# Optimization experiments

Hardware: AMD Instinct MI355X
Metric: run time of the kernel (lower is better)

## Reference

```python
import jax, jax.numpy as jnp
import numpy as np

B, T, D, U = 64, 2048, 256, 256

def hard_sigmoid(x):
    return jnp.clip(0.2 * x + 0.5, 0.0, 1.0)

def setup_inputs() -> dict:
    key = jax.random.key(0)
    k1, k2, k3 = jax.random.split(key, 3)
    x = jax.random.normal(k1, (B, T, D), dtype=jnp.float32)
    kernel = jax.random.normal(k2, (D, 3 * U), dtype=jnp.float32) * (1.0 / np.sqrt(D))
    recurrent_kernel = jax.random.normal(k3, (U, 3 * U), dtype=jnp.float32) * (1.0 / np.sqrt(U))
    bias = jnp.zeros((3 * U,), dtype=jnp.float32)
    return {"x": x, "kernel": kernel, "recurrent_kernel": recurrent_kernel, "bias": bias}

def reference(x, kernel, recurrent_kernel, bias):
    # implementation=0 style: precompute input projections for all timesteps in one big matmul
    # x: [B,T,D], kernel: [D,3U] -> xz/xr/xh each [B,T,U]
    units = recurrent_kernel.shape[0]
    x_proj = jnp.einsum('btd,dh->bth', x, kernel) + bias  # [B,T,3U]
    xz, xr, xh = jnp.split(x_proj, 3, axis=-1)
    Uz = recurrent_kernel[:, :units]
    Ur = recurrent_kernel[:, units:2 * units]
    Uh = recurrent_kernel[:, 2 * units:]

    def step(h, xs):
        xz_t, xr_t, xh_t = xs  # each [B,U]
        z = hard_sigmoid(xz_t + h @ Uz)
        r = hard_sigmoid(xr_t + h @ Ur)
        hh = jnp.tanh(xh_t + (r * h) @ Uh)
        h_new = z * h + (1.0 - z) * hh
        return h_new, None

    h0 = jnp.zeros((x.shape[0], units), dtype=x.dtype)
    # scan over time: move T to leading axis
    xs = (jnp.swapaxes(xz, 0, 1), jnp.swapaxes(xr, 0, 1), jnp.swapaxes(xh, 0, 1))
    h_last, _ = jax.lax.scan(step, h0, xs)
    return h_last  # [B, U] (return_sequences=False)
```

## Files before the change

kernel.cpp:

```cpp
#include <hip/hip_runtime.h>


#define TB 2048
#define NU 256
#define G3 768

typedef __attribute__((ext_vector_type(8))) short bf16x8;
typedef __attribute__((ext_vector_type(4))) float f32x4;

__device__ inline unsigned short f2bf(float f){
  union{float f; unsigned u;} v; v.f = f;
  unsigned r = v.u + 0x7fffu + ((v.u >> 16) & 1u);
  return (unsigned short)(r >> 16);
}
__device__ inline unsigned pk2(float a, float b){
  return (unsigned)f2bf(a) | ((unsigned)f2bf(b) << 16);
}
__device__ inline float bflo(unsigned u){
  union{unsigned u; float f;} v; v.u = u << 16; return v.f;
}
__device__ inline float bfhi(unsigned u){
  union{unsigned u; float f;} v; v.u = u & 0xffff0000u; return v.f;
}
__device__ inline unsigned cvtpk(float a, float b){
  unsigned r;
  asm("v_cvt_pk_bf16_f32 %0, %1, %2" : "=v"(r) : "v"(a), "v"(b));
  return r;
}
__device__ inline float exp2_fast(float x){
#if __has_builtin(__builtin_amdgcn_exp2f)
  return __builtin_amdgcn_exp2f(x);
#else
  float r; asm("v_exp_f32 %0, %1" : "=v"(r) : "v"(x)); return r;
#endif
}

__global__ __launch_bounds__(256) void transpose_k(const float* __restrict__ W,
                                                   const float* __restrict__ R,
                                                   unsigned short* __restrict__ Wt,
                                                   unsigned short* __restrict__ Ut){
  int n = blockIdx.x;
  int k = threadIdx.x;
  if (n < G3) Wt[n*NU + k] = f2bf(W[k*G3 + n]);
  else        Ut[(n-G3)*NU + k] = f2bf(R[k*G3 + (n-G3)]);
}

__global__ __launch_bounds__(256) void proj_k(const float* __restrict__ x,
                                              const unsigned short* __restrict__ Wt,
                                              const float* __restrict__ bias,
                                              unsigned short* __restrict__ XA,
                                              unsigned short* __restrict__ XB){
  __shared__ short As[4096];
  __shared__ short Bs[4096];
  __shared__ short St[4096];
  const int tid  = threadIdx.x;
  const int lane = tid & 63;
  const int wv   = tid >> 6;
  const int wr   = wv >> 1, wc = wv & 1;
  const int q    = lane >> 4, r16 = lane & 15;
  const int tm   = blockIdx.y;
  const int bn   = blockIdx.x;

  f32x4 acc[2][2];
  #pragma unroll
  for (int a=0;a<2;a++)
    #pragma unroll
    for (int b=0;b<2;b++) acc[a][b] = {0.f,0.f,0.f,0.f};

  const int mA = tid >> 2, kq = tid & 3;
  const int kc32 = kq >> 1, q0 = (kq & 1) * 2;

  for (int kc0 = 0; kc0 < 256; kc0 += 64){
    {
      const float* src = x + (size_t)mA*(2048*256) + (size_t)tm*256 + kc0 + kq*16;
      float4 f0 = *(const float4*)(src);
      float4 f1 = *(const float4*)(src+4);
      float4 f2 = *(const float4*)(src+8);
      float4 f3 = *(const float4*)(src+12);
      *(uint2*)&As[kc32*2048 + q0*512     + mA*8 + 0] = make_uint2(pk2(f0.x,f0.y), pk2(f0.z,f0.w));
      *(uint2*)&As[kc32*2048 + q0*512     + mA*8 + 4] = make_uint2(pk2(f1.x,f1.y), pk2(f1.z,f1.w));
      *(uint2*)&As[kc32*2048 + (q0+1)*512 + mA*8 + 0] = make_uint2(pk2(f2.x,f2.y), pk2(f2.z,f2.w));
      *(uint2*)&As[kc32*2048 + (q0+1)*512 + mA*8 + 4] = make_uint2(pk2(f3.x,f3.y), pk2(f3.z,f3.w));
    }
    {
      const unsigned short* srcB = Wt + (size_t)(bn*64 + mA)*256 + kc0 + kq*16;
      uint4 b0v = *(const uint4*)(srcB);
      uint4 b1v = *(const uint4*)(srcB+8);
      *(uint4*)&Bs[kc32*2048 + q0*512     + mA*8] = b0v;
      *(uint4*)&Bs[kc32*2048 + (q0+1)*512 + mA*8] = b1v;
    }
    __syncthreads();
    #pragma unroll
    for (int kk = 0; kk < 2; kk++){
      bf16x8 av[2], bv[2];
      #pragma unroll
      for (int rt=0; rt<2; rt++)
        av[rt] = *(const bf16x8*)&As[kk*2048 + q*512 + (wr*32+rt*16+r16)*8];
      #pragma unroll
      for (int ct=0; ct<2; ct++)
        bv[ct] = *(const bf16x8*)&Bs[kk*2048 + q*512 + (wc*32+ct*16+r16)*8];
      #pragma unroll
      for (int rt=0; rt<2; rt++)
        #pragma unroll
        for (int ct=0; ct<2; ct++)
          acc[rt][ct] = __builtin_amdgcn_mfma_f32_16x16x32_bf16(av[rt], bv[ct], acc[rt][ct], 0,0,0);
    }
    __syncthreads();
  }

  const int csub = (bn < 4) ? 0 : (bn < 8 ? 256 : 512);
  #pragma unroll
  for (int rt=0; rt<2; rt++){
    #pragma unroll
    for (int ct=0; ct<2; ct++){
      int colg = bn*64 + wc*32 + ct*16 + r16;
      float bb = bias[colg];
      int c = colg - csub;
      int wi = (c >> 5) & 1, tt2 = (c >> 4) & 1, r16g = c & 15;
      #pragma unroll
      for (int i=0;i<4;i++){
        int b = wr*32 + rt*16 + q*4 + i;
        int gg = b >> 4, lb = b & 15;
        int lane_ = (lb >> 2)*16 + r16g, ii = lb & 3;
        St[(gg*2+wi)*512 + lane_*8 + tt2*4 + ii] = (short)f2bf(acc[rt][ct][i] + bb);
      }
    }
  }
  __syncthreads();

  #pragma unroll
  for (int it=0; it<2; it++){
    int idx = tid + it*256;
    int chunk = idx >> 6, within = idx & 63;
    int gg = chunk >> 1, wi = chunk & 1;
    int w_ = (bn & 3)*2 + wi;
    uint4 val = *(const uint4*)&St[chunk*512 + within*8];
    if (bn < 8){
      int sel = (bn < 4) ? 0 : 1;
      *((uint4*)XA + ((((size_t)tm*4+gg)*8 + w_)*64 + within)*2 + sel) = val;
    } else {
      *((uint4*)XB + (((size_t)tm*4+gg)*8 + w_)*64 + within) = val;
    }
  }
}

__global__ __launch_bounds__(512, 2) void gru_k(const unsigned short* __restrict__ XA,
                                                const unsigned short* __restrict__ XB,
                                                const unsigned short* __restrict__ Ut,
                                                float* __restrict__ out){
  __shared__ short fb[8192];

  const int tid  = threadIdx.x;
  const int w    = tid >> 6;
  const int lane = tid & 63;
  const int q    = lane >> 4, r16 = lane & 15;
  const int g    = blockIdx.x;
  const int b0   = g * 16;

  const int lswz = (lane & ~3) | ((lane & 3) ^ ((((lane >> 4) & 1) << 1) | ((lane >> 3) & 1)));
  const int ix   = ((r16 >> 3) << 1) | ((lane >> 5) & 1);
  const int wrb  = w*512 + (r16 >> 3)*128 + q*32 + (r16 & 7);

  for (int i = tid; i < 8192; i += 512) fb[i] = 0;

  bf16x8 Uz[2][8], Ur[2][8], Uh[2][8];
  #pragma unroll
  for (int tt=0; tt<2; tt++){
    int cz = w*32 + tt*16 + r16;
    #pragma unroll
    for (int kc=0; kc<8; kc++){
      Uz[tt][kc] = *(const bf16x8*)&Ut[(cz      )*256 + kc*32 + q*8];
      Ur[tt][kc] = *(const bf16x8*)&Ut[(cz + 256)*256 + kc*32 + q*8];
      Uh[tt][kc] = *(const bf16x8*)&Ut[(cz + 512)*256 + kc*32 + q*8];
    }
  }

  float hprev[2][4] = {{0.f,0.f,0.f,0.f},{0.f,0.f,0.f,0.f}};

  const uint4* pA = (const uint4*)XA + ((size_t)(g*8+w)*64 + lane)*2;
  const uint4* pB = (const uint4*)XB + ((size_t)(g*8+w)*64 + lane);

  uint4 xa0 = pA[0], xa1 = pA[1];
  uint4 xb0 = pB[0];
  pA += 4096; pB += 2048;

  __syncthreads();

  #pragma unroll 1
  for (int t = 0; t < TB; t++){
    uint4 na0 = pA[0], na1 = pA[1];
    uint4 nb0 = pB[0];
    pA += 4096; pB += 2048;

    unsigned xw[8] = {xa0.x,xa0.y,xa0.z,xa0.w,xa1.x,xa1.y,xa1.z,xa1.w};

    f32x4 az[2], ar[2];
    #pragma unroll
    for (int tt=0; tt<2; tt++){
      #pragma unroll
      for (int i=0;i<4;i++){
        int s  = tt*4 + i;
        int sr = 8 + s;
        az[tt][i] = (s&1)  ? bfhi(xw[s>>1])  : bflo(xw[s>>1]);
        ar[tt][i] = (sr&1) ? bfhi(xw[sr>>1]) : bflo(xw[sr>>1]);
      }
    }
    #pragma unroll
    for (int kc=0; kc<8; kc++){
      bf16x8 a = *(const bf16x8*)&fb[kc*512 + lswz*8];
      ar[0] = __builtin_amdgcn_mfma_f32_16x16x32_bf16(a, Ur[0][kc], ar[0], 0,0,0);
      ar[1] = __builtin_amdgcn_mfma_f32_16x16x32_bf16(a, Ur[1][kc], ar[1], 0,0,0);
      az[0] = __builtin_amdgcn_mfma_f32_16x16x32_bf16(a, Uz[0][kc], az[0], 0,0,0);
      az[1] = __builtin_amdgcn_mfma_f32_16x16x32_bf16(a, Uz[1][kc], az[1], 0,0,0);
    }
    #pragma unroll
    for (int tt=0; tt<2; tt++){
      #pragma unroll
      for (int i=0;i<4;i++){
        float rr = __builtin_amdgcn_fmed3f(fmaf(0.2f, ar[tt][i], 0.5f), 0.f, 1.f);
        float v  = rr * hprev[tt][i];
        fb[4096 + wrb + tt*256 + ((i^ix)<<3)] = (short)cvtpk(v, v);
      }
    }
    __syncthreads();

    f32x4 ah[2];
    {
      unsigned xwb[4] = {xb0.x,xb0.y,xb0.z,xb0.w};
      #pragma unroll
      for (int ct=0; ct<2; ct++){
        #pragma unroll
        for (int i=0;i<4;i++){
          int s = ct*4 + i;
          ah[ct][i] = (s&1) ? bfhi(xwb[s>>1]) : bflo(xwb[s>>1]);
        }
      }
    }
    #pragma unroll
    for (int kc=0; kc<8; kc++){
      bf16x8 vv = *(const bf16x8*)&fb[4096 + kc*512 + lswz*8];
      ah[0] = __builtin_amdgcn_mfma_f32_16x16x32_bf16(vv, Uh[0][kc], ah[0], 0,0,0);
      ah[1] = __builtin_amdgcn_mfma_f32_16x16x32_bf16(vv, Uh[1][kc], ah[1], 0,0,0);
    }
    float z8[2][4];
    #pragma unroll
    for (int tt=0; tt<2; tt++)
      #pragma unroll
      for (int i=0;i<4;i++)
        z8[tt][i] = __builtin_amdgcn_fmed3f(fmaf(0.2f, az[tt][i], 0.5f), 0.f, 1.f);
    #pragma unroll
    for (int ct=0; ct<2; ct++){
      #pragma unroll
      for (int i=0;i<4;i++){
        float e  = exp2_fast(2.8853900817779268f * ah[ct][i]);
        float rc = __builtin_amdgcn_rcpf(e + 1.f);
        float hh = fmaf(-2.f, rc, 1.f);
        float hn = fmaf(z8[ct][i], hprev[ct][i] - hh, hh);
        hprev[ct][i] = hn;
        fb[wrb + ct*256 + ((i^ix)<<3)] = (short)cvtpk(hn, hn);
      }
    }
    __syncthreads();

    xa0 = na0; xa1 = na1; xb0 = nb0;
  }

  #pragma unroll
  for (int ct=0; ct<2; ct++)
    #pragma unroll
    for (int i=0;i<4;i++)
      out[(size_t)(b0 + q*4 + i)*256 + w*32 + ct*16 + r16] = hprev[ct][i];
}

extern "C" void kernel_launch(void* const* d_in, const int* in_sizes, int n_in,
                              void* d_out, int out_size, void* d_ws, size_t ws_size,
                              hipStream_t stream) {
  (void)in_sizes; (void)n_in; (void)out_size; (void)ws_size;
  const float* x    = (const float*)d_in[0];
  const float* Wk   = (const float*)d_in[1];
  const float* Rk   = (const float*)d_in[2];
  const float* bias = (const float*)d_in[3];
  float* out = (float*)d_out;

  unsigned short* XA = (unsigned short*)d_ws;
  unsigned short* XB = XA + (size_t)2048*32768;
  unsigned short* Wt = XB + (size_t)2048*16384;
  unsigned short* Ut = Wt + (size_t)768*256;

  hipLaunchKernelGGL(transpose_k, dim3(1536),    dim3(256), 0, stream, Wk, Rk, Wt, Ut);
  hipLaunchKernelGGL(proj_k,      dim3(12,2048), dim3(256), 0, stream, x, Wt, bias, XA, XB);
  hipLaunchKernelGGL(gru_k,       dim3(4),       dim3(512), 0, stream, XA, XB, Ut, out);
}
```

Before: 3.256 ms.

## Keep projection weight tile resident in LDS across 16 timesteps per block

The projection kernel now loads the full 64x256 bf16 weight slice into shared memory once and loops over 16 timesteps per block, cutting the grid from 2048 to 128 blocks along time. This removes repeated weight reloads and per-K-chunk syncs and stages all of K for x at once. In exchange it uses much more LDS per block (about 72KB), which lowers occupancy, and it runs fewer, longer blocks. Total runtime is likely dominated by the sequential GRU kernel, so the gain is limited.

```diff
diff --git a/kernel.cpp b/kernel.cpp
--- a/kernel.cpp
+++ b/kernel.cpp
@@ -50,96 +50,106 @@
                                               const float* __restrict__ bias,
                                               unsigned short* __restrict__ XA,
                                               unsigned short* __restrict__ XB){
-  __shared__ short As[4096];
-  __shared__ short Bs[4096];
+  __shared__ short AsAll[16384];
+  __shared__ short BsAll[16384];
   __shared__ short St[4096];
   const int tid  = threadIdx.x;
   const int lane = tid & 63;
   const int wv   = tid >> 6;
   const int wr   = wv >> 1, wc = wv & 1;
   const int q    = lane >> 4, r16 = lane & 15;
-  const int tm   = blockIdx.y;
   const int bn   = blockIdx.x;
-
-  f32x4 acc[2][2];
-  #pragma unroll
-  for (int a=0;a<2;a++)
-    #pragma unroll
-    for (int b=0;b<2;b++) acc[a][b] = {0.f,0.f,0.f,0.f};
+  const int tc   = blockIdx.y;
 
   const int mA = tid >> 2, kq = tid & 3;
   const int kc32 = kq >> 1, q0 = (kq & 1) * 2;
 
-  for (int kc0 = 0; kc0 < 256; kc0 += 64){
-    {
-      const float* src = x + (size_t)mA*(2048*256) + (size_t)tm*256 + kc0 + kq*16;
+  #pragma unroll
+  for (int kc0i = 0; kc0i < 4; kc0i++){
+    const unsigned short* srcB = Wt + (size_t)(bn*64 + mA)*256 + kc0i*64 + kq*16;
+    uint4 b0v = *(const uint4*)(srcB);
+    uint4 b1v = *(const uint4*)(srcB+8);
+    *(uint4*)&BsAll[kc0i*4096 + kc32*2048 + q0*512     + mA*8] = b0v;
+    *(uint4*)&BsAll[kc0i*4096 + kc32*2048 + (q0+1)*512 + mA*8] = b1v;
+  }
+
+  const int csub = (bn < 4) ? 0 : (bn < 8 ? 256 : 512);
+
+  for (int t16 = 0; t16 < 16; t16++){
+    const int tm = tc*16 + t16;
+
+    #pragma unroll
+    for (int kc0i = 0; kc0i < 4; kc0i++){
+      const float* src = x + (size_t)mA*(2048*256) + (size_t)tm*256 + kc0i*64 + kq*16;
       float4 f0 = *(const float4*)(src);
       float4 f1 = *(const float4*)(src+4);
       float4 f2 = *(const float4*)(src+8);
       float4 f3 = *(const float4*)(src+12);
-      *(uint2*)&As[kc32*2048 + q0*512     + mA*8 + 0] = make_uint2(pk2(f0.x,f0.y), pk2(f0.z,f0.w));
-      *(uint2*)&As[kc32*2048 + q0*512     + mA*8 + 4] = make_uint2(pk2(f1.x,f1.y), pk2(f1.z,f1.w));
-      *(uint2*)&As[kc32*2048 + (q0+1)*512 + mA*8 + 0] = make_uint2(pk2(f2.x,f2.y), pk2(f2.z,f2.w));
-      *(uint2*)&As[kc32*2048 + (q0+1)*512 + mA*8 + 4] = make_uint2(pk2(f3.x,f3.y), pk2(f3.z,f3.w));
-    }
-    {
-      const unsigned short* srcB = Wt + (size_t)(bn*64 + mA)*256 + kc0 + kq*16;
-      uint4 b0v = *(const uint4*)(srcB);
-      uint4 b1v = *(const uint4*)(srcB+8);
-      *(uint4*)&Bs[kc32*2048 + q0*512     + mA*8] = b0v;
-      *(uint4*)&Bs[kc32*2048 + (q0+1)*512 + mA*8] = b1v;
-    }
-    __syncthreads();
-    #pragma unroll
-    for (int kk = 0; kk < 2; kk++){
-      bf16x8 av[2], bv[2];
-      #pragma unroll
-      for (int rt=0; rt<2; rt++)
-        av[rt] = *(const bf16x8*)&As[kk*2048 + q*512 + (wr*32+rt*16+r16)*8];
-      #pragma unroll
-      for (int ct=0; ct<2; ct++)
-        bv[ct] = *(const bf16x8*)&Bs[kk*2048 + q*512 + (wc*32+ct*16+r16)*8];
-      #pragma unroll
-      for (int rt=0; rt<2; rt++)
+      *(uint2*)&AsAll[kc0i*4096 + kc32*2048 + q0*512     + mA*8 + 0] = make_uint2(pk2(f0.x,f0.y), pk2(f0.z,f0.w));
+      *(uint2*)&AsAll[kc0i*4096 + kc32*2048 + q0*512     + mA*8 + 4] = make_uint2(pk2(f1.x,f1.y), pk2(f1.z,f1.w));
+      *(uint2*)&AsAll[kc0i*4096 + kc32*2048 + (q0+1)*512 + mA*8 + 0] = make_uint2(pk2(f2.x,f2.y), pk2(f2.z,f2.w));
+      *(uint2*)&AsAll[kc0i*4096 + kc32*2048 + (q0+1)*512 + mA*8 + 4] = make_uint2(pk2(f3.x,f3.y), pk2(f3.z,f3.w));
+    }
+    __syncthreads();
+
+    f32x4 acc[2][2];
+    #pragma unroll
+    for (int a=0;a<2;a++)
+      #pragma unroll
+      for (int b=0;b<2;b++) acc[a][b] = {0.f,0.f,0.f,0.f};
+
+    #pragma unroll
+    for (int kc0i = 0; kc0i < 4; kc0i++){
+      #pragma unroll
+      for (int kk = 0; kk < 2; kk++){
+        bf16x8 av[2], bv[2];
+        #pragma unroll
+        for (int rt=0; rt<2; rt++)
+          av[rt] = *(const bf16x8*)&AsAll[kc0i*4096 + kk*2048 + q*512 + (wr*32+rt*16+r16)*8];
         #pragma unroll
         for (int ct=0; ct<2; ct++)
-          acc[rt][ct] = __builtin_amdgcn_mfma_f32_16x16x32_bf16(av[rt], bv[ct], acc[rt][ct], 0,0,0);
-    }
-    __syncthreads();
-  }
-
-  const int csub = (bn < 4) ? 0 : (bn < 8 ? 256 : 512);
-  #pragma unroll
-  for (int rt=0; rt<2; rt++){
-    #pragma unroll
-    for (int ct=0; ct<2; ct++){
-      int colg = bn*64 + wc*32 + ct*16 + r16;
-      float bb = bias[colg];
-      int c = colg - csub;
-      int wi = (c >> 5) & 1, tt2 = (c >> 4) & 1, r16g = c & 15;
-      #pragma unroll
-      for (int i=0;i<4;i++){
-        int b = wr*32 + rt*16 + q*4 + i;
-        int gg = b >> 4, lb = b & 15;
-        int lane_ = (lb >> 2)*16 + r16g, ii = lb & 3;
-        St[(gg*2+wi)*512 + lane_*8 + tt2*4 + ii] = (short)f2bf(acc[rt][ct][i] + bb);
-      }
-    }
-  }
-  __syncthreads();
-
-  #pragma unroll
-  for (int it=0; it<2; it++){
-    int idx = tid + it*256;
-    int chunk = idx >> 6, within = idx & 63;
-    int gg = chunk >> 1, wi = chunk & 1;
-    int w_ = (bn & 3)*2 + wi;
-    uint4 val = *(const uint4*)&St[chunk*512 + within*8];
-    if (bn < 8){
-      int sel = (bn < 4) ? 0 : 1;
-      *((uint4*)XA + ((((size_t)tm*4+gg)*8 + w_)*64 + within)*2 + sel) = val;
-    } else {
-      *((uint4*)XB + (((size_t)tm*4+gg)*8 + w_)*64 + within) = val;
+          bv[ct] = *(const bf16x8*)&BsAll[kc0i*4096 + kk*2048 + q*512 + (wc*32+ct*16+r16)*8];
+        #pragma unroll
+        for (int rt=0; rt<2; rt++)
+          #pragma unroll
+          for (int ct=0; ct<2; ct++)
+            acc[rt][ct] = __builtin_amdgcn_mfma_f32_16x16x32_bf16(av[rt], bv[ct], acc[rt][ct], 0,0,0);
+      }
+    }
+    __syncthreads();
+
+    #pragma unroll
+    for (int rt=0; rt<2; rt++){
+      #pragma unroll
+      for (int ct=0; ct<2; ct++){
+        int colg = bn*64 + wc*32 + ct*16 + r16;
+        float bb = bias[colg];
+        int c = colg - csub;
+        int wi = (c >> 5) & 1, tt2 = (c >> 4) & 1, r16g = c & 15;
+        #pragma unroll
+        for (int i=0;i<4;i++){
+          int b = wr*32 + rt*16 + q*4 + i;
+          int gg = b >> 4, lb = b & 15;
+          int lane_ = (lb >> 2)*16 + r16g, ii = lb & 3;
+          St[(gg*2+wi)*512 + lane_*8 + tt2*4 + ii] = (short)f2bf(acc[rt][ct][i] + bb);
+        }
+      }
+    }
+    __syncthreads();
+
+    #pragma unroll
+    for (int it=0; it<2; it++){
+      int idx = tid + it*256;
+      int chunk = idx >> 6, within = idx & 63;
+      int gg = chunk >> 1, wi = chunk & 1;
+      int w_ = (bn & 3)*2 + wi;
+      uint4 val = *(const uint4*)&St[chunk*512 + within*8];
+      if (bn < 8){
+        int sel = (bn < 4) ? 0 : 1;
+        *((uint4*)XA + ((((size_t)tm*4+gg)*8 + w_)*64 + within)*2 + sel) = val;
+      } else {
+        *((uint4*)XB + (((size_t)tm*4+gg)*8 + w_)*64 + within) = val;
+      }
     }
   }
 }
@@ -287,7 +297,7 @@
   unsigned short* Wt = XB + (size_t)2048*16384;
   unsigned short* Ut = Wt + (size_t)768*256;
 
-  hipLaunchKernelGGL(transpose_k, dim3(1536),    dim3(256), 0, stream, Wk, Rk, Wt, Ut);
-  hipLaunchKernelGGL(proj_k,      dim3(12,2048), dim3(256), 0, stream, x, Wt, bias, XA, XB);
-  hipLaunchKernelGGL(gru_k,       dim3(4),       dim3(512), 0, stream, XA, XB, Ut, out);
-}
+  hipLaunchKernelGGL(transpose_k, dim3(1536),   dim3(256), 0, stream, Wk, Rk, Wt, Ut);
+  hipLaunchKernelGGL(proj_k,      dim3(12,128), dim3(256), 0, stream, x, Wt, bias, XA, XB);
+  hipLaunchKernelGGL(gru_k,       dim3(4),      dim3(512), 0, stream, XA, XB, Ut, out);
+}
```

Result: no change. 3.302 ms (+1.4%).

## Fuse projection and GRU recurrence into one kernel with per-timestep ready flags

Applied to the files above, without the earlier changes.

Merges the input-projection GEMM and the sequential GRU scan into a single launch. The first 4 blocks run the recurrence and spin on per-timestep atomic counters, while the remaining blocks compute projection tiles and signal completion with release atomics. The aim is to overlap the large projection phase with the latency-bound recurrence instead of running them back to back. In exchange, projection blocks now use 512 threads with half idle, and correctness depends on the 4 recurrent blocks being resident and on projection blocks being scheduled roughly in timestep order.

```diff
diff --git a/kernel.cpp b/kernel.cpp
--- a/kernel.cpp
+++ b/kernel.cpp
@@ -34,121 +34,142 @@
   float r; asm("v_exp_f32 %0, %1" : "=v"(r) : "v"(x)); return r;
 #endif
 }
+__device__ inline void spin_pause(){
+#if __has_builtin(__builtin_amdgcn_s_sleep)
+  __builtin_amdgcn_s_sleep(1);
+#endif
+}
 
 __global__ __launch_bounds__(256) void transpose_k(const float* __restrict__ W,
                                                    const float* __restrict__ R,
                                                    unsigned short* __restrict__ Wt,
-                                                   unsigned short* __restrict__ Ut){
+                                                   unsigned short* __restrict__ Ut,
+                                                   unsigned* __restrict__ cnt){
   int n = blockIdx.x;
   int k = threadIdx.x;
+  int idx = n*256 + k;
+  if (idx < TB) cnt[idx] = 0;
   if (n < G3) Wt[n*NU + k] = f2bf(W[k*G3 + n]);
   else        Ut[(n-G3)*NU + k] = f2bf(R[k*G3 + (n-G3)]);
 }
 
-__global__ __launch_bounds__(256) void proj_k(const float* __restrict__ x,
-                                              const unsigned short* __restrict__ Wt,
-                                              const float* __restrict__ bias,
-                                              unsigned short* __restrict__ XA,
-                                              unsigned short* __restrict__ XB){
+__global__ __launch_bounds__(512, 2) void fused_k(const float* __restrict__ x,
+                                                  const unsigned short* __restrict__ Wt,
+                                                  const float* __restrict__ bias,
+                                                  unsigned short* __restrict__ XA,
+                                                  unsigned short* __restrict__ XB,
+                                                  const unsigned short* __restrict__ Ut,
+                                                  float* __restrict__ out,
+                                                  unsigned* __restrict__ cnt){
+  __shared__ short fb[8192];
   __shared__ short As[4096];
   __shared__ short Bs[4096];
   __shared__ short St[4096];
-  const int tid  = threadIdx.x;
-  const int lane = tid & 63;
-  const int wv   = tid >> 6;
-  const int wr   = wv >> 1, wc = wv & 1;
-  const int q    = lane >> 4, r16 = lane & 15;
-  const int tm   = blockIdx.y;
-  const int bn   = blockIdx.x;
-
-  f32x4 acc[2][2];
-  #pragma unroll
-  for (int a=0;a<2;a++)
-    #pragma unroll
-    for (int b=0;b<2;b++) acc[a][b] = {0.f,0.f,0.f,0.f};
-
-  const int mA = tid >> 2, kq = tid & 3;
-  const int kc32 = kq >> 1, q0 = (kq & 1) * 2;
-
-  for (int kc0 = 0; kc0 < 256; kc0 += 64){
-    {
-      const float* src = x + (size_t)mA*(2048*256) + (size_t)tm*256 + kc0 + kq*16;
-      float4 f0 = *(const float4*)(src);
-      float4 f1 = *(const float4*)(src+4);
-      float4 f2 = *(const float4*)(src+8);
-      float4 f3 = *(const float4*)(src+12);
-      *(uint2*)&As[kc32*2048 + q0*512     + mA*8 + 0] = make_uint2(pk2(f0.x,f0.y), pk2(f0.z,f0.w));
-      *(uint2*)&As[kc32*2048 + q0*512     + mA*8 + 4] = make_uint2(pk2(f1.x,f1.y), pk2(f1.z,f1.w));
-      *(uint2*)&As[kc32*2048 + (q0+1)*512 + mA*8 + 0] = make_uint2(pk2(f2.x,f2.y), pk2(f2.z,f2.w));
-      *(uint2*)&As[kc32*2048 + (q0+1)*512 + mA*8 + 4] = make_uint2(pk2(f3.x,f3.y), pk2(f3.z,f3.w));
-    }
-    {
-      const unsigned short* srcB = Wt + (size_t)(bn*64 + mA)*256 + kc0 + kq*16;
-      uint4 b0v = *(const uint4*)(srcB);
-      uint4 b1v = *(const uint4*)(srcB+8);
-      *(uint4*)&Bs[kc32*2048 + q0*512     + mA*8] = b0v;
-      *(uint4*)&Bs[kc32*2048 + (q0+1)*512 + mA*8] = b1v;
+
+  if (blockIdx.x >= 4){
+    const int pid  = (int)blockIdx.x - 4;
+    const int bn   = pid % 12;
+    const int tm   = pid / 12;
+    const bool act = (threadIdx.x < 256);
+    const int tid  = (int)threadIdx.x & 255;
+    const int lane = tid & 63;
+    const int wv   = tid >> 6;
+    const int wr   = wv >> 1, wc = wv & 1;
+    const int q    = lane >> 4, r16 = lane & 15;
+
+    f32x4 acc[2][2];
+    #pragma unroll
+    for (int a=0;a<2;a++)
+      #pragma unroll
+      for (int b=0;b<2;b++) acc[a][b] = {0.f,0.f,0.f,0.f};
+
+    const int mA = tid >> 2, kq = tid & 3;
+    const int kc32 = kq >> 1, q0 = (kq & 1) * 2;
+
+    for (int kc0 = 0; kc0 < 256; kc0 += 64){
+      if (act){
+        const float* src = x + (size_t)mA*(2048*256) + (size_t)tm*256 + kc0 + kq*16;
+        float4 f0 = *(const float4*)(src);
+        float4 f1 = *(const float4*)(src+4);
+        float4 f2 = *(const float4*)(src+8);
+        float4 f3 = *(const float4*)(src+12);
+        *(uint2*)&As[kc32*2048 + q0*512     + mA*8 + 0] = make_uint2(pk2(f0.x,f0.y), pk2(f0.z,f0.w));
+        *(uint2*)&As[kc32*2048 + q0*512     + mA*8 + 4] = make_uint2(pk2(f1.x,f1.y), pk2(f1.z,f1.w));
+        *(uint2*)&As[kc32*2048 + (q0+1)*512 + mA*8 + 0] = make_uint2(pk2(f2.x,f2.y), pk2(f2.z,f2.w));
+        *(uint2*)&As[kc32*2048 + (q0+1)*512 + mA*8 + 4] = make_uint2(pk2(f3.x,f3.y), pk2(f3.z,f3.w));
+        const unsigned short* srcB = Wt + (size_t)(bn*64 + mA)*256 + kc0 + kq*16;
+        uint4 b0v = *(const uint4*)(srcB);
+        uint4 b1v = *(const uint4*)(srcB+8);
+        *(uint4*)&Bs[kc32*2048 + q0*512     + mA*8] = b0v;
+        *(uint4*)&Bs[kc32*2048 + (q0+1)*512 + mA*8] = b1v;
+      }
+      __syncthreads();
+      if (act){
+        #pragma unroll
+        for (int kk = 0; kk < 2; kk++){
+          bf16x8 av[2], bv[2];
+          #pragma unroll
+          for (int rt=0; rt<2; rt++)
+            av[rt] = *(const bf16x8*)&As[kk*2048 + q*512 + (wr*32+rt*16+r16)*8];
+          #pragma unroll
+          for (int ct=0; ct<2; ct++)
+            bv[ct] = *(const bf16x8*)&Bs[kk*2048 + q*512 + (wc*32+ct*16+r16)*8];
+          #pragma unroll
+          for (int rt=0; rt<2; rt++)
+            #pragma unroll
+            for (int ct=0; ct<2; ct++)
+              acc[rt][ct] = __builtin_amdgcn_mfma_f32_16x16x32_bf16(av[rt], bv[ct], acc[rt][ct], 0,0,0);
+        }
+      }
+      __syncthreads();
+    }
+
+    const int csub = (bn < 4) ? 0 : (bn < 8 ? 256 : 512);
+    if (act){
+      #pragma unroll
+      for (int rt=0; rt<2; rt++){
+        #pragma unroll
+        for (int ct=0; ct<2; ct++){
+          int colg = bn*64 + wc*32 + ct*16 + r16;
+          float bb = bias[colg];
+          int c = colg - csub;
+          int wi = (c >> 5) & 1, tt2 = (c >> 4) & 1, r16g = c & 15;
+          #pragma unroll
+          for (int i=0;i<4;i++){
+            int b = wr*32 + rt*16 + q*4 + i;
+            int gg = b >> 4, lb = b & 15;
+            int lane_ = (lb >> 2)*16 + r16g, ii = lb & 3;
+            St[(gg*2+wi)*512 + lane_*8 + tt2*4 + ii] = (short)f2bf(acc[rt][ct][i] + bb);
+          }
+        }
+      }
     }
     __syncthreads();
-    #pragma unroll
-    for (int kk = 0; kk < 2; kk++){
-      bf16x8 av[2], bv[2];
-      #pragma unroll
-      for (int rt=0; rt<2; rt++)
-        av[rt] = *(const bf16x8*)&As[kk*2048 + q*512 + (wr*32+rt*16+r16)*8];
-      #pragma unroll
-      for (int ct=0; ct<2; ct++)
-        bv[ct] = *(const bf16x8*)&Bs[kk*2048 + q*512 + (wc*32+ct*16+r16)*8];
-      #pragma unroll
-      for (int rt=0; rt<2; rt++)
-        #pragma unroll
-        for (int ct=0; ct<2; ct++)
-          acc[rt][ct] = __builtin_amdgcn_mfma_f32_16x16x32_bf16(av[rt], bv[ct], acc[rt][ct], 0,0,0);
-    }
+
+    if (act){
+      #pragma unroll
+      for (int it=0; it<2; it++){
+        int idx = tid + it*256;
+        int chunk = idx >> 6, within = idx & 63;
+        int gg = chunk >> 1, wi = chunk & 1;
+        int w_ = (bn & 3)*2 + wi;
+        uint4 val = *(const uint4*)&St[chunk*512 + within*8];
+        if (bn < 8){
+          int sel = (bn < 4) ? 0 : 1;
+          *((uint4*)XA + ((((size_t)tm*4+gg)*8 + w_)*64 + within)*2 + sel) = val;
+        } else {
+          *((uint4*)XB + (((size_t)tm*4+gg)*8 + w_)*64 + within) = val;
+        }
+      }
+    }
+    __threadfence();
     __syncthreads();
+    if (threadIdx.x == 0)
+      __hip_atomic_fetch_add(&cnt[tm], 1u, __ATOMIC_RELEASE, __HIP_MEMORY_SCOPE_AGENT);
+    return;
   }
 
-  const int csub = (bn < 4) ? 0 : (bn < 8 ? 256 : 512);
-  #pragma unroll
-  for (int rt=0; rt<2; rt++){
-    #pragma unroll
-    for (int ct=0; ct<2; ct++){
-      int colg = bn*64 + wc*32 + ct*16 + r16;
-      float bb = bias[colg];
-      int c = colg - csub;
-      int wi = (c >> 5) & 1, tt2 = (c >> 4) & 1, r16g = c & 15;
-      #pragma unroll
-      for (int i=0;i<4;i++){
-        int b = wr*32 + rt*16 + q*4 + i;
-        int gg = b >> 4, lb = b & 15;
-        int lane_ = (lb >> 2)*16 + r16g, ii = lb & 3;
-        St[(gg*2+wi)*512 + lane_*8 + tt2*4 + ii] = (short)f2bf(acc[rt][ct][i] + bb);
-      }
-    }
-  }
-  __syncthreads();
-
-  #pragma unroll
-  for (int it=0; it<2; it++){
-    int idx = tid + it*256;
-    int chunk = idx >> 6, within = idx & 63;
-    int gg = chunk >> 1, wi = chunk & 1;
-    int w_ = (bn & 3)*2 + wi;
-    uint4 val = *(const uint4*)&St[chunk*512 + within*8];
-    if (bn < 8){
-      int sel = (bn < 4) ? 0 : 1;
-      *((uint4*)XA + ((((size_t)tm*4+gg)*8 + w_)*64 + within)*2 + sel) = val;
-    } else {
-      *((uint4*)XB + (((size_t)tm*4+gg)*8 + w_)*64 + within) = val;
-    }
-  }
-}
-
-__global__ __launch_bounds__(512, 2) void gru_k(const unsigned short* __restrict__ XA,
-                                                const unsigned short* __restrict__ XB,
-                                                const unsigned short* __restrict__ Ut,
-                                                float* __restrict__ out){
-  __shared__ short fb[8192];
+  __builtin_amdgcn_s_setprio(1);
 
   const int tid  = threadIdx.x;
   const int w    = tid >> 6;
@@ -180,17 +201,28 @@
   const uint4* pA = (const uint4*)XA + ((size_t)(g*8+w)*64 + lane)*2;
   const uint4* pB = (const uint4*)XB + ((size_t)(g*8+w)*64 + lane);
 
+  unsigned flagv;
+  do { flagv = __hip_atomic_load(&cnt[0], __ATOMIC_ACQUIRE, __HIP_MEMORY_SCOPE_AGENT);
+       if (flagv < 12u) spin_pause(); } while (flagv < 12u);
   uint4 xa0 = pA[0], xa1 = pA[1];
   uint4 xb0 = pB[0];
   pA += 4096; pB += 2048;
+  flagv = __hip_atomic_load(&cnt[1], __ATOMIC_ACQUIRE, __HIP_MEMORY_SCOPE_AGENT);
 
   __syncthreads();
 
   #pragma unroll 1
   for (int t = 0; t < TB; t++){
+    const int tn = (t+1 < TB) ? t+1 : TB-1;
+    if (flagv < 12u){
+      do { flagv = __hip_atomic_load(&cnt[tn], __ATOMIC_ACQUIRE, __HIP_MEMORY_SCOPE_AGENT);
+           if (flagv < 12u) spin_pause(); } while (flagv < 12u);
+    }
     uint4 na0 = pA[0], na1 = pA[1];
     uint4 nb0 = pB[0];
     pA += 4096; pB += 2048;
+    const int tn2 = (t+2 < TB) ? t+2 : TB-1;
+    flagv = __hip_atomic_load(&cnt[tn2], __ATOMIC_ACQUIRE, __HIP_MEMORY_SCOPE_AGENT);
 
     unsigned xw[8] = {xa0.x,xa0.y,xa0.z,xa0.w,xa1.x,xa1.y,xa1.z,xa1.w};
 
@@ -286,8 +318,8 @@
   unsigned short* XB = XA + (size_t)2048*32768;
   unsigned short* Wt = XB + (size_t)2048*16384;
   unsigned short* Ut = Wt + (size_t)768*256;
-
-  hipLaunchKernelGGL(transpose_k, dim3(1536),    dim3(256), 0, stream, Wk, Rk, Wt, Ut);
-  hipLaunchKernelGGL(proj_k,      dim3(12,2048), dim3(256), 0, stream, x, Wt, bias, XA, XB);
-  hipLaunchKernelGGL(gru_k,       dim3(4),       dim3(512), 0, stream, XA, XB, Ut, out);
-}
+  unsigned*       cnt = (unsigned*)(Ut + (size_t)768*256);
+
+  hipLaunchKernelGGL(transpose_k, dim3(1536),  dim3(256), 0, stream, Wk, Rk, Wt, Ut, cnt);
+  hipLaunchKernelGGL(fused_k,     dim3(24580), dim3(512), 0, stream, x, Wt, bias, XA, XB, Ut, out, cnt);
+}
```

New measurement: 11.26 ms. 246% more time.
